# Performance work log

Hardware: AMD Instinct MI355X
Metric: run time of the kernel (lower is better)

## Reference

```python
import jax, jax.numpy as jnp
import numpy as np

D = 256      # dim
H = 8        # num_heads
HD = D // H  # head dim
P = 256      # patch_size
B = 4        # num clouds
L = 32768    # points per cloud (divisible by P)
N = B * L
MLP = int(D * 2.0)
PEH = max(32, D // 4)
EPS = 1e-5


def setup_inputs() -> dict:
    key = jax.random.key(0)
    ks = jax.random.split(key, 20)
    s = 0.02
    w = lambda k, shp: jax.random.normal(k, shp, jnp.float32) * s
    inp = {
        "feats": jax.random.normal(ks[0], (N, D), jnp.float32),
        "coord": jax.random.uniform(ks[1], (N, 3), jnp.float32),
        "lengths": jnp.full((B,), L, jnp.int32),
        # CoordPositionalEncoding: Linear(3,PEH) -> ReLU -> Linear(PEH,D)
        "pe_w1": w(ks[2], (3, PEH)), "pe_b1": jnp.zeros((PEH,), jnp.float32),
        "pe_w2": w(ks[3], (PEH, D)), "pe_b2": jnp.zeros((D,), jnp.float32),
        "pre_g": jnp.ones((D,), jnp.float32), "pre_b": jnp.zeros((D,), jnp.float32),
        # block: norm1 + MHA + norm2 + MLP
        "n1_g": jnp.ones((D,), jnp.float32), "n1_b": jnp.zeros((D,), jnp.float32),
        "wqkv": w(ks[4], (D, 3 * D)), "bqkv": jnp.zeros((3 * D,), jnp.float32),
        "wo": w(ks[5], (D, D)), "bo": jnp.zeros((D,), jnp.float32),
        "n2_g": jnp.ones((D,), jnp.float32), "n2_b": jnp.zeros((D,), jnp.float32),
        "m_w1": w(ks[6], (D, MLP)), "m_b1": jnp.zeros((MLP,), jnp.float32),
        "m_w2": w(ks[7], (MLP, D)), "m_b2": jnp.zeros((D,), jnp.float32),
        # global_gate: Linear(2D,D)->ReLU->Linear(D,D)->Sigmoid
        "gg_w1": w(ks[8], (2 * D, D)), "gg_b1": jnp.zeros((D,), jnp.float32),
        "gg_w2": w(ks[9], (D, D)), "gg_b2": jnp.zeros((D,), jnp.float32),
        # fuse: Linear(2D,D)->ReLU->Linear(D,D)
        "f_w1": w(ks[10], (2 * D, D)), "f_b1": jnp.zeros((D,), jnp.float32),
        "f_w2": w(ks[11], (D, D)), "f_b2": jnp.zeros((D,), jnp.float32),
    }
    return inp


def _ln(x, g, b):
    m = x.mean(-1, keepdims=True)
    v = jnp.mean((x - m) ** 2, -1, keepdims=True)
    return (x - m) * jax.lax.rsqrt(v + EPS) * g + b


def _sgca(feats, coord, lengths,
          pe_w1, pe_b1, pe_w2, pe_b2, pre_g, pre_b,
          n1_g, n1_b, wqkv, bqkv, wo, bo, n2_g, n2_b,
          m_w1, m_b1, m_w2, m_b2,
          gg_w1, gg_b1, gg_w2, gg_b2, f_w1, f_b1, f_w2, f_b2):
    Bn = lengths.shape[0]
    Ln = feats.shape[0] // Bn  # equal-length clouds

    def cloud(f, c):  # f: [L, D], c: [L, 3]
        # positional encoding (per-cloud centered / max-abs scaled coords)
        cc = c - c.mean(0, keepdims=True)
        scale = jnp.clip(jnp.abs(cc).max(0, keepdims=True), 1e-6)
        pe = jax.nn.relu((cc / scale) @ pe_w1 + pe_b1) @ pe_w2 + pe_b2
        x = _ln(f + pe, pre_g, pre_b)
        # serialization order from min-max normalized coords
        cn = c - c.min(0, keepdims=True)
        cn = cn / jnp.clip(cn.max(0, keepdims=True), 1e-6)
        key = cn[:, 0] + 2.17 * cn[:, 1] + 3.31 * cn[:, 2]
        order = jnp.argsort(key)
        xs = x[order].reshape(-1, P, D)  # [NP, P, D] block-diagonal windows
        # attention block (pre-norm MHA + residual)
        h = _ln(xs, n1_g, n1_b)
        qkv = h @ wqkv + bqkv
        q = qkv[..., :D].reshape(-1, P, H, HD)
        k = qkv[..., D:2 * D].reshape(-1, P, H, HD)
        v = qkv[..., 2 * D:].reshape(-1, P, H, HD)
        scores = jnp.einsum('nphd,nqhd->nhpq', q, k) / np.sqrt(HD).astype(np.float32)
        a = jax.nn.softmax(scores, axis=-1)
        o = jnp.einsum('nhpq,nqhd->nphd', a, v).reshape(-1, P, D)
        xs = xs + (o @ wo + bo)
        # MLP + residual
        xs = xs + (jax.nn.gelu(_ln(xs, n2_g, n2_b) @ m_w1 + m_b1, approximate=False) @ m_w2 + m_b2)
        # undo serialization
        xo = xs.reshape(-1, D)[jnp.argsort(order)]
        # global token gate/fuse
        gt = jnp.broadcast_to(xo.mean(0, keepdims=True), xo.shape)
        gate = jax.nn.sigmoid(jax.nn.relu(jnp.concatenate([f, gt], -1) @ gg_w1 + gg_b1) @ gg_w2 + gg_b2)
        fused = jax.nn.relu(jnp.concatenate([xo, gt], -1) @ f_w1 + f_b1) @ f_w2 + f_b2
        return f + gate * fused

    out = jax.vmap(cloud)(feats.reshape(Bn, Ln, D), coord.reshape(Bn, Ln, 3))
    return out.reshape(-1, D)


def reference(feats, coord, lengths,
              pe_w1, pe_b1, pe_w2, pe_b2, pre_g, pre_b,
              n1_g, n1_b, wqkv, bqkv, wo, bo, n2_g, n2_b,
              m_w1, m_b1, m_w2, m_b2,
              gg_w1, gg_b1, gg_w2, gg_b2, f_w1, f_b1, f_w2, f_b2):
    return _sgca(feats, coord, lengths,
                 pe_w1, pe_b1, pe_w2, pe_b2, pre_g, pre_b,
                 n1_g, n1_b, wqkv, bqkv, wo, bo, n2_g, n2_b,
                 m_w1, m_b1, m_w2, m_b2,
                 gg_w1, gg_b1, gg_w2, gg_b2, f_w1, f_b1, f_w2, f_b2)
```

## Files before the change

### kernel.cpp

```cpp
#include <hip/hip_runtime.h>
#include <hip/hip_bf16.h>
#include <math.h>

#define D_DIM 256
#define NHEAD 8
#define HDIM 32
#define PATCH 256
#define NCLOUD 4
#define LPC 32768
#define NTOT (NCLOUD * LPC)
#define MLPD 512
#define PEHID 64
#define LN_EPS 1e-5f
#define NCHUNK 4
#define CROWS (NTOT / NCHUNK)

typedef unsigned long long u64;
typedef unsigned short u16;
typedef short bf16x8 __attribute__((ext_vector_type(8)));
typedef float f32x4 __attribute__((ext_vector_type(4)));

__device__ __forceinline__ u16 f2bf(float x) {
  unsigned u = __float_as_uint(x);
  u += 0x7fffu + ((u >> 16) & 1u);
  return (u16)(u >> 16);
}
__device__ __forceinline__ float bf2f(u16 u) {
  return __uint_as_float(((unsigned)u) << 16);
}

__device__ __forceinline__ void gload_lds16(const u16* g, u16* l) {
  __builtin_amdgcn_global_load_lds((const __attribute__((address_space(1))) void*)g,
                                   (__attribute__((address_space(3))) void*)l, 16, 0, 0);
}

__global__ __launch_bounds__(256) void stats_kernel(const float* __restrict__ coord,
                                                    float* __restrict__ stats) {
  const int c = blockIdx.x, t = threadIdx.x;
  float sm[3] = {0.f, 0.f, 0.f};
  float mn[3] = {1e30f, 1e30f, 1e30f};
  float mx[3] = {-1e30f, -1e30f, -1e30f};
  const float* cp = coord + (size_t)c * LPC * 3;
  for (int i = t; i < LPC; i += 256) {
#pragma unroll
    for (int a = 0; a < 3; a++) {
      float v = cp[(size_t)i * 3 + a];
      sm[a] += v;
      mn[a] = fminf(mn[a], v);
      mx[a] = fmaxf(mx[a], v);
    }
  }
  __shared__ float sb[256];
  float rsum[3], rmn[3], rmx[3];
#pragma unroll
  for (int a = 0; a < 3; a++) {
    sb[t] = sm[a]; __syncthreads();
    for (int s = 128; s > 0; s >>= 1) { if (t < s) sb[t] += sb[t + s]; __syncthreads(); }
    rsum[a] = sb[0]; __syncthreads();
    sb[t] = mn[a]; __syncthreads();
    for (int s = 128; s > 0; s >>= 1) { if (t < s) sb[t] = fminf(sb[t], sb[t + s]); __syncthreads(); }
    rmn[a] = sb[0]; __syncthreads();
    sb[t] = mx[a]; __syncthreads();
    for (int s = 128; s > 0; s >>= 1) { if (t < s) sb[t] = fmaxf(sb[t], sb[t + s]); __syncthreads(); }
    rmx[a] = sb[0]; __syncthreads();
  }
  if (t == 0) {
    float* st = stats + c * 16;
#pragma unroll
    for (int a = 0; a < 3; a++) {
      float mean = rsum[a] / (float)LPC;
      st[a] = mean;
      st[3 + a] = fmaxf(fmaxf(rmx[a] - mean, mean - rmn[a]), 1e-6f);
      st[6 + a] = rmn[a];
      st[9 + a] = fmaxf(rmx[a] - rmn[a], 1e-6f);
    }
  }
}

__global__ __launch_bounds__(256) void key_kernel(const float* __restrict__ coord,
                                                  const float* __restrict__ stats,
                                                  u64* __restrict__ keys) {
#pragma clang fp contract(off)
  const int g = blockIdx.x * 256 + threadIdx.x;
  const int c = g >> 15;
  const float* st = stats + c * 16;
  float k0 = (coord[(size_t)g * 3 + 0] - st[6]) / st[9];
  float k1 = (coord[(size_t)g * 3 + 1] - st[7]) / st[10];
  float k2 = (coord[(size_t)g * 3 + 2] - st[8]) / st[11];
  float key = k0 + 2.17f * k1;
  key = key + 3.31f * k2;
  keys[g] = ((u64)__float_as_uint(key) << 32) | (unsigned)(g & (LPC - 1));
}

__global__ __launch_bounds__(1024) void sort_local_kernel(u64* __restrict__ keys) {
  __shared__ u64 s[4096];
  const int base = blockIdx.x * 4096;
  const int t = threadIdx.x;
  for (int i = t; i < 4096; i += 1024) s[i] = keys[base + i];
  __syncthreads();
  for (int k = 2; k <= 4096; k <<= 1) {
    for (int j = k >> 1; j > 0; j >>= 1) {
      for (int p = t; p < 2048; p += 1024) {
        int i = ((p & ~(j - 1)) << 1) | (p & (j - 1));
        int l = i | j;
        bool asc = (((base + i) & (LPC - 1)) & k) == 0;
        u64 a = s[i], bb = s[l];
        if (asc ? (a > bb) : (a < bb)) { s[i] = bb; s[l] = a; }
      }
      __syncthreads();
    }
  }
  for (int i = t; i < 4096; i += 1024) keys[base + i] = s[i];
}

__global__ __launch_bounds__(256) void sort_global_kernel(u64* __restrict__ keys, int k, int j) {
  int p = blockIdx.x * 256 + threadIdx.x;
  int i = ((p & ~(j - 1)) << 1) | (p & (j - 1));
  int l = i | j;
  bool asc = ((i & (LPC - 1)) & k) == 0;
  u64 a = keys[i], b = keys[l];
  if (asc ? (a > b) : (a < b)) { keys[i] = b; keys[l] = a; }
}

__global__ __launch_bounds__(1024) void sort_finish_kernel(u64* __restrict__ keys, int k) {
  __shared__ u64 s[4096];
  const int base = blockIdx.x * 4096;
  const int t = threadIdx.x;
  for (int i = t; i < 4096; i += 1024) s[i] = keys[base + i];
  __syncthreads();
  for (int j = 2048; j > 0; j >>= 1) {
    for (int p = t; p < 2048; p += 1024) {
      int i = ((p & ~(j - 1)) << 1) | (p & (j - 1));
      int l = i | j;
      bool asc = (((base + i) & (LPC - 1)) & k) == 0;
      u64 a = s[i], bb = s[l];
      if (asc ? (a > bb) : (a < bb)) { s[i] = bb; s[l] = a; }
    }
    __syncthreads();
  }
  for (int i = t; i < 4096; i += 1024) keys[base + i] = s[i];
}

__global__ __launch_bounds__(256) void rank_kernel(const u64* __restrict__ keys,
                                                   int* __restrict__ order,
                                                   int* __restrict__ rank) {
  const int g = blockIdx.x * 256 + threadIdx.x;
  const int src = (int)(unsigned)(keys[g] & 0xffffffffULL) + (g & ~(LPC - 1));
  order[g] = src;
  rank[src] = g;
}

__global__ __launch_bounds__(256) void wtrans_kernel(const float* __restrict__ src,
                                                     u16* __restrict__ dst, int R, int C) {
  __shared__ float t[32][33];
  const int bx = blockIdx.x * 32, by = blockIdx.y * 32;
  const int lc = threadIdx.x & 31, lr = threadIdx.x >> 5;
  for (int i = 0; i < 32; i += 8) t[lr + i][lc] = src[(size_t)(by + lr + i) * C + bx + lc];
  __syncthreads();
  for (int i = 0; i < 32; i += 8)
    dst[(size_t)(bx + lr + i) * R + by + lc] = f2bf(t[lc][lr + i]);
}

__global__ __launch_bounds__(256) void h_kernel(const float* __restrict__ coord,
                                                const float* __restrict__ stats,
                                                const float* __restrict__ pw1,
                                                const float* __restrict__ pb1,
                                                u16* __restrict__ H) {
  const int idx = blockIdx.x * 256 + threadIdx.x;
  const int row = idx >> 6, j = idx & 63;
  const int c = row >> 15;
  const float* st = stats + c * 16;
  float s0 = (coord[(size_t)row * 3 + 0] - st[0]) / st[3];
  float s1 = (coord[(size_t)row * 3 + 1] - st[1]) / st[4];
  float s2 = (coord[(size_t)row * 3 + 2] - st[2]) / st[5];
  float h = pb1[j] + s0 * pw1[j] + s1 * pw1[64 + j] + s2 * pw1[128 + j];
  H[idx] = f2bf(fmaxf(h, 0.f));
}

__global__ __launch_bounds__(256) void add_ln2_kernel(const float* __restrict__ feats,
                                                      const u16* __restrict__ pe,
                                                      const int* __restrict__ rank,
                                                      const float* __restrict__ g0,
                                                      const float* __restrict__ b0,
                                                      const float* __restrict__ g1,
                                                      const float* __restrict__ b1,
                                                      float* __restrict__ xs,
                                                      u16* __restrict__ ln1out) {
  const int row = blockIdx.x * 4 + (threadIdx.x >> 6);
  const int lane = threadIdx.x & 63;
  float4 f = *(const float4*)(feats + (size_t)row * 256 + lane * 4);
  ushort4 p = *(const ushort4*)(pe + (size_t)row * 256 + lane * 4);
  float v0 = f.x + bf2f(p.x), v1 = f.y + bf2f(p.y);
  float v2 = f.z + bf2f(p.z), v3 = f.w + bf2f(p.w);
  float s = v0 + v1 + v2 + v3;
#pragma unroll
  for (int o = 32; o > 0; o >>= 1) s += __shfl_xor(s, o);
  float mean = s * (1.f / 256.f);
  float d0 = v0 - mean, d1 = v1 - mean, d2 = v2 - mean, d3 = v3 - mean;
  float ss = d0 * d0 + d1 * d1 + d2 * d2 + d3 * d3;
#pragma unroll
  for (int o = 32; o > 0; o >>= 1) ss += __shfl_xor(ss, o);
  float inv = 1.f / sqrtf(ss * (1.f / 256.f) + LN_EPS);
  float4 gv = *(const float4*)(g0 + lane * 4);
  float4 bv = *(const float4*)(b0 + lane * 4);
  const int dst = rank[row];
  float y0 = d0 * inv * gv.x + bv.x, y1 = d1 * inv * gv.y + bv.y;
  float y2 = d2 * inv * gv.z + bv.z, y3 = d3 * inv * gv.w + bv.w;
  float4 o4 = {y0, y1, y2, y3};
  *(float4*)(xs + (size_t)dst * 256 + lane * 4) = o4;
  float s2s = y0 + y1 + y2 + y3;
#pragma unroll
  for (int o = 32; o > 0; o >>= 1) s2s += __shfl_xor(s2s, o);
  float mean2 = s2s * (1.f / 256.f);
  float e0 = y0 - mean2, e1 = y1 - mean2, e2 = y2 - mean2, e3 = y3 - mean2;
  float ss2 = e0 * e0 + e1 * e1 + e2 * e2 + e3 * e3;
#pragma unroll
  for (int o = 32; o > 0; o >>= 1) ss2 += __shfl_xor(ss2, o);
  float inv2 = 1.f / sqrtf(ss2 * (1.f / 256.f) + LN_EPS);
  float4 g1v = *(const float4*)(g1 + lane * 4);
  float4 b1v = *(const float4*)(b1 + lane * 4);
  ushort4 h4;
  h4.x = f2bf(e0 * inv2 * g1v.x + b1v.x); h4.y = f2bf(e1 * inv2 * g1v.y + b1v.y);
  h4.z = f2bf(e2 * inv2 * g1v.z + b1v.z); h4.w = f2bf(e3 * inv2 * g1v.w + b1v.w);
  *(ushort4*)(ln1out + (size_t)dst * 256 + lane * 4) = h4;
}

template <int K, int ACT, int MODE, bool EXTRA>
__global__ __launch_bounds__(256, 4) void mfma_gemm(const u16* __restrict__ A,
                                                    const u16* __restrict__ Wt,
                                                    const float* __restrict__ bias,
                                                    const float* __restrict__ extra,
                                                    void* __restrict__ Cout, int Ko) {
  __shared__ __align__(16) u16 Al[128 * 32];
  __shared__ __align__(16) u16 Bl[128 * 32];
  const int tid = threadIdx.x;
  const int lane = tid & 63, wave = tid >> 6;
  const int wr = wave >> 1, wc = wave & 1;
  const int l15 = lane & 15, l4 = lane >> 4;
  const size_t row0 = (size_t)blockIdx.y * 128;
  const int col0 = blockIdx.x * 128;
  const int q0 = wave * 64 + lane;
  const int q1 = q0 + 256;
  const u16* gA0 = A + (row0 + (q0 >> 2)) * K + (q0 & 3) * 8;
  const u16* gA1 = A + (row0 + (q1 >> 2)) * K + (q1 & 3) * 8;
  const u16* gB0 = Wt + (size_t)(col0 + (q0 >> 2)) * K + (q0 & 3) * 8;
  const u16* gB1 = Wt + (size_t)(col0 + (q1 >> 2)) * K + (q1 & 3) * 8;
  u16* lA0 = Al + wave * 512;
  u16* lA1 = Al + 2048 + wave * 512;
  u16* lB0 = Bl + wave * 512;
  u16* lB1 = Bl + 2048 + wave * 512;
  f32x4 acc[4][4];
#pragma unroll
  for (int i = 0; i < 4; i++)
#pragma unroll
    for (int j = 0; j < 4; j++) acc[i][j] = f32x4{0.f, 0.f, 0.f, 0.f};
#pragma unroll 1
  for (int k0 = 0; k0 < K; k0 += 32) {
    gload_lds16(gA0 + k0, lA0);
    gload_lds16(gA1 + k0, lA1);
    gload_lds16(gB0 + k0, lB0);
    gload_lds16(gB1 + k0, lB1);
    __syncthreads();
    bf16x8 af[4], bfr[4];
#pragma unroll
    for (int rb = 0; rb < 4; rb++)
      af[rb] = *(const bf16x8*)&Al[(wr * 64 + rb * 16 + l15) * 32 + l4 * 8];
#pragma unroll
    for (int cb = 0; cb < 4; cb++)
      bfr[cb] = *(const bf16x8*)&Bl[(wc * 64 + cb * 16 + l15) * 32 + l4 * 8];
#pragma unroll
    for (int rb = 0; rb < 4; rb++)
#pragma unroll
      for (int cb = 0; cb < 4; cb++)
        acc[rb][cb] = __builtin_amdgcn_mfma_f32_16x16x32_bf16(af[rb], bfr[cb], acc[rb][cb], 0, 0, 0);
    __syncthreads();
  }
#pragma unroll
  for (int rb = 0; rb < 4; rb++)
#pragma unroll
    for (int cb = 0; cb < 4; cb++)
#pragma unroll
      for (int r = 0; r < 4; r++) {
        size_t row = row0 + wr * 64 + rb * 16 + l4 * 4 + r;
        int col = col0 + wc * 64 + cb * 16 + l15;
        float v = acc[rb][cb][r] + bias[col];
        if (EXTRA) v += extra[((int)(row >> 15)) * 256 + col];
        if (ACT == 1) v = fmaxf(v, 0.f);
        else if (ACT == 2) v = 0.5f * v * (1.f + erff(v * 0.70710678118654752440f));
        else if (ACT == 3) v = 1.f / (1.f + __expf(-v));
        size_t o = row * (size_t)Ko + col;
        if (MODE == 0) ((float*)Cout)[o] = v;
        else if (MODE == 1) ((float*)Cout)[o] += v;
        else ((u16*)Cout)[o] = f2bf(v);
      }
}

template <int K, int EPI>
__global__ __launch_bounds__(256, 3) void mfma_row_gemm(const u16* __restrict__ A,
                                                        const u16* __restrict__ Wt,
                                                        const float* __restrict__ bias,
                                                        float* __restrict__ xs,
                                                        u16* __restrict__ hout,
                                                        const int* __restrict__ order,
                                                        const float* __restrict__ g,
                                                        const float* __restrict__ b) {
  __shared__ __align__(16) u16 Al[64 * 32];
  __shared__ __align__(16) u16 Bl[256 * 32];
  __shared__ float reds[2][4][64];
  const int tid = threadIdx.x;
  const int lane = tid & 63, wave = tid >> 6;
  const int l15 = lane & 15, l4 = lane >> 4;
  const size_t row0 = (size_t)blockIdx.x * 64;
  const u16* gA = A + (row0 + (tid >> 2)) * K + (tid & 3) * 8;
  u16* lA = Al + wave * 512;
  const u16* gB[4];
  u16* lB[4];
#pragma unroll
  for (int s = 0; s < 4; s++) {
    int q = s * 256 + tid;
    gB[s] = Wt + (size_t)(q >> 2) * K + (q & 3) * 8;
    lB[s] = Bl + s * 2048 + wave * 512;
  }
  f32x4 acc[4][4];
#pragma unroll
  for (int i = 0; i < 4; i++)
#pragma unroll
    for (int j = 0; j < 4; j++) acc[i][j] = f32x4{0.f, 0.f, 0.f, 0.f};
#pragma unroll 1
  for (int k0 = 0; k0 < K; k0 += 32) {
    gload_lds16(gA + k0, lA);
#pragma unroll
    for (int s = 0; s < 4; s++) gload_lds16(gB[s] + k0, lB[s]);
    __syncthreads();
    bf16x8 af[4], bfr[4];
#pragma unroll
    for (int rb = 0; rb < 4; rb++)
      af[rb] = *(const bf16x8*)&Al[(rb * 16 + l15) * 32 + l4 * 8];
#pragma unroll
    for (int cb = 0; cb < 4; cb++)
      bfr[cb] = *(const bf16x8*)&Bl[(wave * 64 + cb * 16 + l15) * 32 + l4 * 8];
#pragma unroll
    for (int rb = 0; rb < 4; rb++)
#pragma unroll
      for (int cb = 0; cb < 4; cb++)
        acc[rb][cb] = __builtin_amdgcn_mfma_f32_16x16x32_bf16(af[rb], bfr[cb], acc[rb][cb], 0, 0, 0);
    __syncthreads();
  }
#pragma unroll
  for (int rb = 0; rb < 4; rb++)
#pragma unroll
    for (int cb = 0; cb < 4; cb++)
#pragma unroll
      for (int r = 0; r < 4; r++) {
        size_t row = row0 + rb * 16 + l4 * 4 + r;
        int col = wave * 64 + cb * 16 + l15;
        size_t o = row * 256 + col;
        float t = xs[o] + acc[rb][cb][r] + bias[col];
        xs[o] = t;
        acc[rb][cb][r] = t;
      }
  if (EPI == 1) {
    float ps[4][4];
#pragma unroll
    for (int rb = 0; rb < 4; rb++)
#pragma unroll
      for (int r = 0; r < 4; r++) {
        float v = acc[rb][0][r] + acc[rb][1][r] + acc[rb][2][r] + acc[rb][3][r];
#pragma unroll
        for (int oo = 1; oo < 16; oo <<= 1) v += __shfl_xor(v, oo);
        ps[rb][r] = v;
      }
    if (l15 == 0)
#pragma unroll
      for (int rb = 0; rb < 4; rb++)
#pragma unroll
        for (int r = 0; r < 4; r++) reds[0][wave][rb * 16 + l4 * 4 + r] = ps[rb][r];
    __syncthreads();
    float mean[4][4];
#pragma unroll
    for (int rb = 0; rb < 4; rb++)
#pragma unroll
      for (int r = 0; r < 4; r++) {
        int ri = rb * 16 + l4 * 4 + r;
        mean[rb][r] = (reds[0][0][ri] + reds[0][1][ri] + reds[0][2][ri] + reds[0][3][ri]) *
                      (1.f / 256.f);
      }
#pragma unroll
    for (int rb = 0; rb < 4; rb++)
#pragma unroll
      for (int r = 0; r < 4; r++) {
        float d0 = acc[rb][0][r] - mean[rb][r], d1 = acc[rb][1][r] - mean[rb][r];
        float d2 = acc[rb][2][r] - mean[rb][r], d3 = acc[rb][3][r] - mean[rb][r];
        float v = d0 * d0 + d1 * d1 + d2 * d2 + d3 * d3;
#pragma unroll
        for (int oo = 1; oo < 16; oo <<= 1) v += __shfl_xor(v, oo);
        ps[rb][r] = v;
      }
    if (l15 == 0)
#pragma unroll
      for (int rb = 0; rb < 4; rb++)
#pragma unroll
        for (int r = 0; r < 4; r++) reds[1][wave][rb * 16 + l4 * 4 + r] = ps[rb][r];
    __syncthreads();
#pragma unroll
    for (int rb = 0; rb < 4; rb++)
#pragma unroll
      for (int r = 0; r < 4; r++) {
        int ri = rb * 16 + l4 * 4 + r;
        float var = (reds[1][0][ri] + reds[1][1][ri] + reds[1][2][ri] + reds[1][3][ri]) *
                    (1.f / 256.f);
        float inv = 1.f / sqrtf(var + LN_EPS);
        size_t row = row0 + ri;
#pragma unroll
        for (int cb = 0; cb < 4; cb++) {
          int col = wave * 64 + cb * 16 + l15;
          hout[row * 256 + col] =
              f2bf((acc[rb][cb][r] - mean[rb][r]) * inv * g[col] + b[col]);
        }
      }
  } else {
#pragma unroll
    for (int rb = 0; rb < 4; rb++)
#pragma unroll
      for (int r = 0; r < 4; r++) {
        size_t row = row0 + rb * 16 + l4 * 4 + r;
        size_t dst = (size_t)order[row];
#pragma unroll
        for (int cb = 0; cb < 4; cb++) {
          int col = wave * 64 + cb * 16 + l15;
          hout[dst * 256 + col] = f2bf(acc[rb][cb][r]);
        }
      }
  }
}

__global__ __launch_bounds__(256, 2) void tail_kernel(
    const float* __restrict__ feats, const u16* __restrict__ xobf,
    const u16* __restrict__ ggw1T, const u16* __restrict__ fw1T,
    const u16* __restrict__ ggw2T, const u16* __restrict__ fw2T,
    const float* __restrict__ ggt, const float* __restrict__ fgt,
    const float* __restrict__ b1g, const float* __restrict__ b1f,
    const float* __restrict__ b2g, const float* __restrict__ b2f,
    float* __restrict__ out) {
  __shared__ __align__(16) u16 g1l[32 * 264];
  __shared__ __align__(16) u16 u1l[32 * 264];
  __shared__ __align__(16) u16 Bst[2][256 * 32];
  __shared__ __align__(16) u16 Ast[2][32 * 32];
  const int tid = threadIdx.x;
  const int lane = tid & 63, wave = tid >> 6;
  const int l15 = lane & 15, l4 = lane >> 4;
  const size_t row0 = (size_t)blockIdx.x * 32;
  const int cloud = (int)(row0 >> 15);
  f32x4 acc[2][4];

#pragma unroll
  for (int i = 0; i < 2; i++)
#pragma unroll
    for (int j = 0; j < 4; j++) acc[i][j] = f32x4{0.f, 0.f, 0.f, 0.f};
#pragma unroll 1
  for (int k0 = 0; k0 < 256; k0 += 64) {
    __syncthreads();
#pragma unroll
    for (int h = 0; h < 2; h++) {
#pragma unroll
      for (int s = 0; s < 4; s++) {
        int q = s * 256 + tid;
        gload_lds16(ggw1T + (size_t)(q >> 2) * 256 + k0 + h * 32 + (q & 3) * 8,
                    &Bst[h][0] + s * 2048 + wave * 512);
      }
      int r = tid >> 3, c4 = (tid & 7) * 4;
      float4 v = *(const float4*)(feats + (row0 + r) * 256 + k0 + h * 32 + c4);
      ushort4 o4; o4.x = f2bf(v.x); o4.y = f2bf(v.y); o4.z = f2bf(v.z); o4.w = f2bf(v.w);
      *(ushort4*)&Ast[h][r * 32 + c4] = o4;
    }
    __syncthreads();
#pragma unroll
    for (int h = 0; h < 2; h++) {
      bf16x8 af[2];
#pragma unroll
      for (int rb = 0; rb < 2; rb++)
        af[rb] = *(const bf16x8*)&Ast[h][(rb * 16 + l15) * 32 + l4 * 8];
#pragma unroll
      for (int cb = 0; cb < 4; cb++) {
        bf16x8 bf = *(const bf16x8*)&Bst[h][(wave * 64 + cb * 16 + l15) * 32 + l4 * 8];
#pragma unroll
        for (int rb = 0; rb < 2; rb++)
          acc[rb][cb] = __builtin_amdgcn_mfma_f32_16x16x32_bf16(af[rb], bf, acc[rb][cb], 0, 0, 0);
      }
    }
  }
#pragma unroll
  for (int rb = 0; rb < 2; rb++)
#pragma unroll
    for (int cb = 0; cb < 4; cb++)
#pragma unroll
      for (int r = 0; r < 4; r++) {
        int row = rb * 16 + l4 * 4 + r;
        int col = wave * 64 + cb * 16 + l15;
        float v = acc[rb][cb][r] + b1g[col] + ggt[cloud * 256 + col];
        g1l[row * 264 + col] = f2bf(fmaxf(v, 0.f));
      }
#pragma unroll
  for (int i = 0; i < 2; i++)
#pragma unroll
    for (int j = 0; j < 4; j++) acc[i][j] = f32x4{0.f, 0.f, 0.f, 0.f};
#pragma unroll 1
  for (int k0 = 0; k0 < 256; k0 += 64) {
    __syncthreads();
#pragma unroll
    for (int h = 0; h < 2; h++) {
#pragma unroll
      for (int s = 0; s < 4; s++) {
        int q = s * 256 + tid;
        gload_lds16(fw1T + (size_t)(q >> 2) * 256 + k0 + h * 32 + (q & 3) * 8,
                    &Bst[h][0] + s * 2048 + wave * 512);
      }
      if (tid < 128) {
        int q = tid;
        gload_lds16(xobf + (row0 + (q >> 2)) * 256 + k0 + h * 32 + (q & 3) * 8,
                    &Ast[h][0] + wave * 512);
      }
    }
    __syncthreads();
#pragma unroll
    for (int h = 0; h < 2; h++) {
      bf16x8 af[2];
#pragma unroll
      for (int rb = 0; rb < 2; rb++)
        af[rb] = *(const bf16x8*)&Ast[h][(rb * 16 + l15) * 32 + l4 * 8];
#pragma unroll
      for (int cb = 0; cb < 4; cb++) {
        bf16x8 bf = *(const bf16x8*)&Bst[h][(wave * 64 + cb * 16 + l15) * 32 + l4 * 8];
#pragma unroll
        for (int rb = 0; rb < 2; rb++)
          acc[rb][cb] = __builtin_amdgcn_mfma_f32_16x16x32_bf16(af[rb], bf, acc[rb][cb], 0, 0, 0);
      }
    }
  }
#pragma unroll
  for (int rb = 0; rb < 2; rb++)
#pragma unroll
    for (int cb = 0; cb < 4; cb++)
#pragma unroll
      for (int r = 0; r < 4; r++) {
        int row = rb * 16 + l4 * 4 + r;
        int col = wave * 64 + cb * 16 + l15;
        float v = acc[rb][cb][r] + b1f[col] + fgt[cloud * 256 + col];
        u1l[row * 264 + col] = f2bf(fmaxf(v, 0.f));
      }
#pragma unroll
  for (int i = 0; i < 2; i++)
#pragma unroll
    for (int j = 0; j < 4; j++) acc[i][j] = f32x4{0.f, 0.f, 0.f, 0.f};
#pragma unroll 1
  for (int k0 = 0; k0 < 256; k0 += 64) {
    __syncthreads();
#pragma unroll
    for (int h = 0; h < 2; h++)
#pragma unroll
      for (int s = 0; s < 4; s++) {
        int q = s * 256 + tid;
        gload_lds16(ggw2T + (size_t)(q >> 2) * 256 + k0 + h * 32 + (q & 3) * 8,
                    &Bst[h][0] + s * 2048 + wave * 512);
      }
    __syncthreads();
#pragma unroll
    for (int h = 0; h < 2; h++) {
      bf16x8 af[2];
#pragma unroll
      for (int rb = 0; rb < 2; rb++)
        af[rb] = *(const bf16x8*)&g1l[(rb * 16 + l15) * 264 + k0 + h * 32 + l4 * 8];
#pragma unroll
      for (int cb = 0; cb < 4; cb++) {
        bf16x8 bf = *(const bf16x8*)&Bst[h][(wave * 64 + cb * 16 + l15) * 32 + l4 * 8];
#pragma unroll
        for (int rb = 0; rb < 2; rb++)
          acc[rb][cb] = __builtin_amdgcn_mfma_f32_16x16x32_bf16(af[rb], bf, acc[rb][cb], 0, 0, 0);
      }
    }
  }
  float sg[2][4][4];
#pragma unroll
  for (int rb = 0; rb < 2; rb++)
#pragma unroll
    for (int cb = 0; cb < 4; cb++)
#pragma unroll
      for (int r = 0; r < 4; r++) {
        int col = wave * 64 + cb * 16 + l15;
        sg[rb][cb][r] = 1.f / (1.f + __expf(-(acc[rb][cb][r] + b2g[col])));
      }
#pragma unroll
  for (int i = 0; i < 2; i++)
#pragma unroll
    for (int j = 0; j < 4; j++) acc[i][j] = f32x4{0.f, 0.f, 0.f, 0.f};
#pragma unroll 1
  for (int k0 = 0; k0 < 256; k0 += 64) {
    __syncthreads();
#pragma unroll
    for (int h = 0; h < 2; h++)
#pragma unroll
      for (int s = 0; s < 4; s++) {
        int q = s * 256 + tid;
        gload_lds16(fw2T + (size_t)(q >> 2) * 256 + k0 + h * 32 + (q & 3) * 8,
                    &Bst[h][0] + s * 2048 + wave * 512);
      }
    __syncthreads();
#pragma unroll
    for (int h = 0; h < 2; h++) {
      bf16x8 af[2];
#pragma unroll
      for (int rb = 0; rb < 2; rb++)
        af[rb] = *(const bf16x8*)&u1l[(rb * 16 + l15) * 264 + k0 + h * 32 + l4 * 8];
#pragma unroll
      for (int cb = 0; cb < 4; cb++) {
        bf16x8 bf = *(const bf16x8*)&Bst[h][(wave * 64 + cb * 16 + l15) * 32 + l4 * 8];
#pragma unroll
        for (int rb = 0; rb < 2; rb++)
          acc[rb][cb] = __builtin_amdgcn_mfma_f32_16x16x32_bf16(af[rb], bf, acc[rb][cb], 0, 0, 0);
      }
    }
  }
#pragma unroll
  for (int rb = 0; rb < 2; rb++)
#pragma unroll
    for (int cb = 0; cb < 4; cb++)
#pragma unroll
      for (int r = 0; r < 4; r++) {
        size_t row = row0 + rb * 16 + l4 * 4 + r;
        int col = wave * 64 + cb * 16 + l15;
        size_t o = row * 256 + col;
        out[o] = feats[o] + sg[rb][cb][r] * (acc[rb][cb][r] + b2f[col]);
      }
}

__global__ __launch_bounds__(256, 3) void attn_mfma_kernel(const u16* __restrict__ qkv,
                                                           u16* __restrict__ ao) {
  __shared__ __align__(16) u16 VT[32 * 264];
  __shared__ __align__(16) u16 Pl[4][16 * 264];
  const int w = blockIdx.x, h = blockIdx.y;
  const int tid = threadIdx.x;
  const int lane = tid & 63, wave = tid >> 6;
  const int l15 = lane & 15, l4 = lane >> 4;
  const size_t base = (size_t)w * PATCH;
  {
    const u16* vrow = qkv + (base + tid) * 768 + 512 + h * HDIM;
#pragma unroll
    for (int d4 = 0; d4 < 8; d4++) {
      ushort4 v4 = *(const ushort4*)(vrow + d4 * 4);
      VT[(d4 * 4 + 0) * 264 + tid] = v4.x;
      VT[(d4 * 4 + 1) * 264 + tid] = v4.y;
      VT[(d4 * 4 + 2) * 264 + tid] = v4.z;
      VT[(d4 * 4 + 3) * 264 + tid] = v4.w;
    }
  }
  __syncthreads();
  u16* Pw = &Pl[wave][0];
  const float scale = 0.17677669529663687f;
  const f32x4 zero = {0.f, 0.f, 0.f, 0.f};
  for (int qt = 0; qt < 4; qt++) {
    const int qbase = wave * 64 + qt * 16;
    bf16x8 qf = *(const bf16x8*)(qkv + (base + qbase + l15) * 768 + h * HDIM + l4 * 8);
    f32x4 s[16];
#pragma unroll
    for (int kt = 0; kt < 16; kt++) {
      bf16x8 kf = *(const bf16x8*)(qkv + (base + kt * 16 + l15) * 768 + 256 + h * HDIM + l4 * 8);
      s[kt] = __builtin_amdgcn_mfma_f32_16x16x32_bf16(kf, qf, zero, 0, 0, 0);
    }
    float m = -1e30f;
#pragma unroll
    for (int kt = 0; kt < 16; kt++)
#pragma unroll
      for (int r = 0; r < 4; r++) { s[kt][r] *= scale; m = fmaxf(m, s[kt][r]); }
    m = fmaxf(m, __shfl_xor(m, 16));
    m = fmaxf(m, __shfl_xor(m, 32));
    float lsum = 0.f;
#pragma unroll
    for (int kt = 0; kt < 16; kt++) {
      float p0 = __expf(s[kt][0] - m), p1 = __expf(s[kt][1] - m);
      float p2 = __expf(s[kt][2] - m), p3 = __expf(s[kt][3] - m);
      lsum += (p0 + p1) + (p2 + p3);
      ushort4 pw4;
      pw4.x = f2bf(p0); pw4.y = f2bf(p1); pw4.z = f2bf(p2); pw4.w = f2bf(p3);
      *(ushort4*)&Pw[l15 * 264 + kt * 16 + l4 * 4] = pw4;
    }
    lsum += __shfl_xor(lsum, 16);
    lsum += __shfl_xor(lsum, 32);
    f32x4 o0 = zero, o1 = zero;
#pragma unroll
    for (int kc = 0; kc < 8; kc++) {
      bf16x8 pf = *(const bf16x8*)&Pw[l15 * 264 + kc * 32 + l4 * 8];
      bf16x8 va = *(const bf16x8*)&VT[l15 * 264 + kc * 32 + l4 * 8];
      bf16x8 vb = *(const bf16x8*)&VT[(16 + l15) * 264 + kc * 32 + l4 * 8];
      o0 = __builtin_amdgcn_mfma_f32_16x16x32_bf16(va, pf, o0, 0, 0, 0);
      o1 = __builtin_amdgcn_mfma_f32_16x16x32_bf16(vb, pf, o1, 0, 0, 0);
    }
    float inv = 1.f / lsum;
    u16* op = ao + (base + qbase + l15) * D_DIM + h * HDIM;
    ushort4 w0, w1;
    w0.x = f2bf(o0[0] * inv); w0.y = f2bf(o0[1] * inv);
    w0.z = f2bf(o0[2] * inv); w0.w = f2bf(o0[3] * inv);
    w1.x = f2bf(o1[0] * inv); w1.y = f2bf(o1[1] * inv);
    w1.z = f2bf(o1[2] * inv); w1.w = f2bf(o1[3] * inv);
    *(ushort4*)(op + l4 * 4) = w0;
    *(ushort4*)(op + 16 + l4 * 4) = w1;
  }
}

__global__ __launch_bounds__(256) void gt_partial_kernel(const float* __restrict__ xs,
                                                         float* __restrict__ part) {
  const int s = blockIdx.x, c = blockIdx.y;
  const int t = threadIdx.x;
  float acc = 0.f;
  const size_t base = (size_t)c * LPC + (size_t)s * 256;
  for (int r = 0; r < 256; r++) acc += xs[(base + r) * D_DIM + t];
  part[(size_t)(c * 128 + s) * D_DIM + t] = acc;
}

__global__ __launch_bounds__(256) void gt_reduce_kernel(const float* __restrict__ part,
                                                        float* __restrict__ gt) {
  const int c = blockIdx.x, t = threadIdx.x;
  float s = 0.f;
  for (int i = 0; i < 128; i++) s += part[(size_t)(c * 128 + i) * D_DIM + t];
  gt[c * D_DIM + t] = s * (1.f / (float)LPC);
}

__global__ __launch_bounds__(256) void pervec_kernel(const float* __restrict__ gt,
                                                     const float* __restrict__ ggw1,
                                                     const float* __restrict__ fw1,
                                                     float* __restrict__ ggt,
                                                     float* __restrict__ fgt) {
  const int c = blockIdx.x, which = blockIdx.y;
  const int t = threadIdx.x;
  const float* W = which ? fw1 : ggw1;
  float* o = which ? fgt : ggt;
  __shared__ float g[D_DIM];
  g[t] = gt[c * D_DIM + t];
  __syncthreads();
  float acc = 0.f;
#pragma unroll 8
  for (int k = 0; k < D_DIM; k++) acc += g[k] * W[(size_t)(256 + k) * D_DIM + t];
  o[c * D_DIM + t] = acc;
}

extern "C" void kernel_launch(void* const* d_in, const int* in_sizes, int n_in,
                              void* d_out, int out_size, void* d_ws, size_t ws_size,
                              hipStream_t stream) {
  const float* feats = (const float*)d_in[0];
  const float* coord = (const float*)d_in[1];
  const float* pe_w1 = (const float*)d_in[3];
  const float* pe_b1 = (const float*)d_in[4];
  const float* pe_w2 = (const float*)d_in[5];
  const float* pe_b2 = (const float*)d_in[6];
  const float* pre_g = (const float*)d_in[7];
  const float* pre_b = (const float*)d_in[8];
  const float* n1_g = (const float*)d_in[9];
  const float* n1_b = (const float*)d_in[10];
  const float* wqkv = (const float*)d_in[11];
  const float* bqkv = (const float*)d_in[12];
  const float* wo = (const float*)d_in[13];
  const float* bo = (const float*)d_in[14];
  const float* n2_g = (const float*)d_in[15];
  const float* n2_b = (const float*)d_in[16];
  const float* m_w1 = (const float*)d_in[17];
  const float* m_b1 = (const float*)d_in[18];
  const float* m_w2 = (const float*)d_in[19];
  const float* m_b2 = (const float*)d_in[20];
  const float* gg_w1 = (const float*)d_in[21];
  const float* gg_b1 = (const float*)d_in[22];
  const float* gg_w2 = (const float*)d_in[23];
  const float* gg_b2 = (const float*)d_in[24];
  const float* f_w1 = (const float*)d_in[25];
  const float* f_b1 = (const float*)d_in[26];
  const float* f_w2 = (const float*)d_in[27];
  const float* f_b2 = (const float*)d_in[28];
  float* out = (float*)d_out;

  char* ws = (char*)d_ws;
  float* xs = (float*)(ws);
  u16* hbuf = (u16*)(ws + 134217728);
  u16* pebuf = (u16*)(ws + 201326592);
  u16* qkvchunk = (u16*)(ws + 201326592);
  u16* aochunk = (u16*)(ws + 251658240);
  u16* tbuf = (u16*)(ws + 268435456);
  u16* Hbuf = (u16*)(ws + 268435456);
  u16* xobf = (u16*)(ws + 201326592);
  size_t off = 301989888;
  u64* keybuf = (u64*)(ws + off); off += (size_t)NTOT * 8;
  int* orderbuf = (int*)(ws + off); off += (size_t)NTOT * 4;
  int* rankbuf = (int*)(ws + off); off += (size_t)NTOT * 4;
  float* statsbuf = (float*)(ws + off); off += 4096;
  float* gtpart = (float*)(ws + off); off += (size_t)NCLOUD * 128 * D_DIM * 4;
  float* gtbuf = (float*)(ws + off); off += 4096;
  float* ggtbuf = (float*)(ws + off); off += 4096;
  float* fgtbuf = (float*)(ws + off); off += 4096;
  u16* wqkvT = (u16*)(ws + off); off += 768 * 256 * 2;
  u16* woT = (u16*)(ws + off); off += 256 * 256 * 2;
  u16* mw1T = (u16*)(ws + off); off += 512 * 256 * 2;
  u16* mw2T = (u16*)(ws + off); off += 256 * 512 * 2;
  u16* ggw1T = (u16*)(ws + off); off += 256 * 256 * 2;
  u16* ggw2T = (u16*)(ws + off); off += 256 * 256 * 2;
  u16* fw1T = (u16*)(ws + off); off += 256 * 256 * 2;
  u16* fw2T = (u16*)(ws + off); off += 256 * 256 * 2;
  u16* pw2T = (u16*)(ws + off); off += 64 * 256 * 2;

  stats_kernel<<<NCLOUD, 256, 0, stream>>>(coord, statsbuf);
  key_kernel<<<NTOT / 256, 256, 0, stream>>>(coord, statsbuf, keybuf);
  sort_local_kernel<<<NTOT / 4096, 1024, 0, stream>>>(keybuf);
  for (int k = 8192; k <= 32768; k <<= 1) {
    for (int j = k >> 1; j >= 4096; j >>= 1)
      sort_global_kernel<<<NTOT / 512, 256, 0, stream>>>(keybuf, k, j);
    sort_finish_kernel<<<NTOT / 4096, 1024, 0, stream>>>(keybuf, k);
  }
  rank_kernel<<<NTOT / 256, 256, 0, stream>>>(keybuf, orderbuf, rankbuf);
  wtrans_kernel<<<dim3(24, 8), 256, 0, stream>>>(wqkv, wqkvT, 256, 768);
  wtrans_kernel<<<dim3(8, 8), 256, 0, stream>>>(wo, woT, 256, 256);
  wtrans_kernel<<<dim3(16, 8), 256, 0, stream>>>(m_w1, mw1T, 256, 512);
  wtrans_kernel<<<dim3(8, 16), 256, 0, stream>>>(m_w2, mw2T, 512, 256);
  wtrans_kernel<<<dim3(8, 8), 256, 0, stream>>>(gg_w1, ggw1T, 256, 256);
  wtrans_kernel<<<dim3(8, 8), 256, 0, stream>>>(gg_w2, ggw2T, 256, 256);
  wtrans_kernel<<<dim3(8, 8), 256, 0, stream>>>(f_w1, fw1T, 256, 256);
  wtrans_kernel<<<dim3(8, 8), 256, 0, stream>>>(f_w2, fw2T, 256, 256);
  wtrans_kernel<<<dim3(8, 2), 256, 0, stream>>>(pe_w2, pw2T, 64, 256);
  h_kernel<<<NTOT * 64 / 256, 256, 0, stream>>>(coord, statsbuf, pe_w1, pe_b1, Hbuf);
  mfma_gemm<64, 0, 2, false><<<dim3(2, NTOT / 128), 256, 0, stream>>>(
      Hbuf, pw2T, pe_b2, nullptr, pebuf, 256);
  add_ln2_kernel<<<NTOT / 4, 256, 0, stream>>>(feats, pebuf, rankbuf, pre_g, pre_b,
                                               n1_g, n1_b, xs, hbuf);
  for (int ch = 0; ch < NCHUNK; ch++) {
    const size_t ro = (size_t)ch * CROWS;
    mfma_gemm<256, 0, 2, false><<<dim3(6, CROWS / 128), 256, 0, stream>>>(
        hbuf + ro * 256, wqkvT, bqkv, nullptr, qkvchunk, 768);
    attn_mfma_kernel<<<dim3(CROWS / PATCH, NHEAD), 256, 0, stream>>>(qkvchunk, aochunk);
    mfma_row_gemm<256, 1><<<CROWS / 64, 256, 0, stream>>>(
        aochunk, woT, bo, xs + ro * 256, hbuf + ro * 256, nullptr, n2_g, n2_b);
  }
  for (int ch = 0; ch < NCHUNK; ch++) {
    const size_t ro = (size_t)ch * CROWS;
    mfma_gemm<256, 2, 2, false><<<dim3(MLPD / 128, CROWS / 128), 256, 0, stream>>>(
        hbuf + ro * 256, mw1T, m_b1, nullptr, tbuf, 512);
    mfma_row_gemm<512, 2><<<CROWS / 64, 256, 0, stream>>>(
        tbuf, mw2T, m_b2, xs + ro * 256, xobf, orderbuf + ro, nullptr, nullptr);
  }
  gt_partial_kernel<<<dim3(128, NCLOUD), 256, 0, stream>>>(xs, gtpart);
  gt_reduce_kernel<<<NCLOUD, 256, 0, stream>>>(gtpart, gtbuf);
  pervec_kernel<<<dim3(NCLOUD, 2), 256, 0, stream>>>(gtbuf, gg_w1, f_w1, ggtbuf, fgtbuf);
  tail_kernel<<<NTOT / 32, 256, 0, stream>>>(feats, xobf, ggw1T, fw1T, ggw2T, fw2T,
                                             ggtbuf, fgtbuf, gg_b1, f_b1, gg_b2, f_b2, out);
  (void)in_sizes; (void)n_in; (void)out_size; (void)ws_size;
}
```

Measured before the change: 1.345 ms.

## Fuse PE GEMM with LayerNorms, enlarge sort tiles, fold global-mean partials into MLP epilogue

The positional-encoding GEMM now runs inside a row kernel whose epilogue adds feats and the bias and applies both LayerNorms before scattering, so the bf16 PE intermediate is never written or re-read. The bitonic sort uses 8192-element shared-memory tiles, which removes several global merge passes and kernel launches. Column sums for the global token are computed in the MLP output GEMM epilogue, replacing the separate pass over xs. In exchange the sort kernels use 64KB of LDS per block, and the fused PE kernel does strided scalar epilogue stores and carries extra register pressure.

Measured after the change: 1.353 ms. No clear change (+0.5%).

```diff
diff --git a/kernel.cpp b/kernel.cpp
--- a/kernel.cpp
+++ b/kernel.cpp
@@ -92,15 +92,15 @@
   keys[g] = ((u64)__float_as_uint(key) << 32) | (unsigned)(g & (LPC - 1));
 }
 
-__global__ __launch_bounds__(1024) void sort_local_kernel(u64* __restrict__ keys) {
-  __shared__ u64 s[4096];
-  const int base = blockIdx.x * 4096;
+__global__ __launch_bounds__(1024) void sort_local8_kernel(u64* __restrict__ keys) {
+  __shared__ u64 s[8192];
+  const int base = blockIdx.x * 8192;
   const int t = threadIdx.x;
-  for (int i = t; i < 4096; i += 1024) s[i] = keys[base + i];
-  __syncthreads();
-  for (int k = 2; k <= 4096; k <<= 1) {
+  for (int i = t; i < 8192; i += 1024) s[i] = keys[base + i];
+  __syncthreads();
+  for (int k = 2; k <= 8192; k <<= 1) {
     for (int j = k >> 1; j > 0; j >>= 1) {
-      for (int p = t; p < 2048; p += 1024) {
+      for (int p = t; p < 4096; p += 1024) {
         int i = ((p & ~(j - 1)) << 1) | (p & (j - 1));
         int l = i | j;
         bool asc = (((base + i) & (LPC - 1)) & k) == 0;
@@ -110,7 +110,7 @@
       __syncthreads();
     }
   }
-  for (int i = t; i < 4096; i += 1024) keys[base + i] = s[i];
+  for (int i = t; i < 8192; i += 1024) keys[base + i] = s[i];
 }
 
 __global__ __launch_bounds__(256) void sort_global_kernel(u64* __restrict__ keys, int k, int j) {
@@ -122,14 +122,14 @@
   if (asc ? (a > b) : (a < b)) { keys[i] = b; keys[l] = a; }
 }
 
-__global__ __launch_bounds__(1024) void sort_finish_kernel(u64* __restrict__ keys, int k) {
-  __shared__ u64 s[4096];
-  const int base = blockIdx.x * 4096;
+__global__ __launch_bounds__(1024) void sort_finish8_kernel(u64* __restrict__ keys, int k) {
+  __shared__ u64 s[8192];
+  const int base = blockIdx.x * 8192;
   const int t = threadIdx.x;
-  for (int i = t; i < 4096; i += 1024) s[i] = keys[base + i];
-  __syncthreads();
-  for (int j = 2048; j > 0; j >>= 1) {
-    for (int p = t; p < 2048; p += 1024) {
+  for (int i = t; i < 8192; i += 1024) s[i] = keys[base + i];
+  __syncthreads();
+  for (int j = 4096; j > 0; j >>= 1) {
+    for (int p = t; p < 4096; p += 1024) {
       int i = ((p & ~(j - 1)) << 1) | (p & (j - 1));
       int l = i | j;
       bool asc = (((base + i) & (LPC - 1)) & k) == 0;
@@ -138,7 +138,7 @@
     }
     __syncthreads();
   }
-  for (int i = t; i < 4096; i += 1024) keys[base + i] = s[i];
+  for (int i = t; i < 8192; i += 1024) keys[base + i] = s[i];
 }
 
 __global__ __launch_bounds__(256) void rank_kernel(const u64* __restrict__ keys,
@@ -177,52 +177,182 @@
   H[idx] = f2bf(fmaxf(h, 0.f));
 }
 
-__global__ __launch_bounds__(256) void add_ln2_kernel(const float* __restrict__ feats,
-                                                      const u16* __restrict__ pe,
-                                                      const int* __restrict__ rank,
-                                                      const float* __restrict__ g0,
-                                                      const float* __restrict__ b0,
-                                                      const float* __restrict__ g1,
-                                                      const float* __restrict__ b1,
-                                                      float* __restrict__ xs,
-                                                      u16* __restrict__ ln1out) {
-  const int row = blockIdx.x * 4 + (threadIdx.x >> 6);
-  const int lane = threadIdx.x & 63;
-  float4 f = *(const float4*)(feats + (size_t)row * 256 + lane * 4);
-  ushort4 p = *(const ushort4*)(pe + (size_t)row * 256 + lane * 4);
-  float v0 = f.x + bf2f(p.x), v1 = f.y + bf2f(p.y);
-  float v2 = f.z + bf2f(p.z), v3 = f.w + bf2f(p.w);
-  float s = v0 + v1 + v2 + v3;
-#pragma unroll
-  for (int o = 32; o > 0; o >>= 1) s += __shfl_xor(s, o);
-  float mean = s * (1.f / 256.f);
-  float d0 = v0 - mean, d1 = v1 - mean, d2 = v2 - mean, d3 = v3 - mean;
-  float ss = d0 * d0 + d1 * d1 + d2 * d2 + d3 * d3;
-#pragma unroll
-  for (int o = 32; o > 0; o >>= 1) ss += __shfl_xor(ss, o);
-  float inv = 1.f / sqrtf(ss * (1.f / 256.f) + LN_EPS);
-  float4 gv = *(const float4*)(g0 + lane * 4);
-  float4 bv = *(const float4*)(b0 + lane * 4);
-  const int dst = rank[row];
-  float y0 = d0 * inv * gv.x + bv.x, y1 = d1 * inv * gv.y + bv.y;
-  float y2 = d2 * inv * gv.z + bv.z, y3 = d3 * inv * gv.w + bv.w;
-  float4 o4 = {y0, y1, y2, y3};
-  *(float4*)(xs + (size_t)dst * 256 + lane * 4) = o4;
-  float s2s = y0 + y1 + y2 + y3;
-#pragma unroll
-  for (int o = 32; o > 0; o >>= 1) s2s += __shfl_xor(s2s, o);
-  float mean2 = s2s * (1.f / 256.f);
-  float e0 = y0 - mean2, e1 = y1 - mean2, e2 = y2 - mean2, e3 = y3 - mean2;
-  float ss2 = e0 * e0 + e1 * e1 + e2 * e2 + e3 * e3;
-#pragma unroll
-  for (int o = 32; o > 0; o >>= 1) ss2 += __shfl_xor(ss2, o);
-  float inv2 = 1.f / sqrtf(ss2 * (1.f / 256.f) + LN_EPS);
-  float4 g1v = *(const float4*)(g1 + lane * 4);
-  float4 b1v = *(const float4*)(b1 + lane * 4);
-  ushort4 h4;
-  h4.x = f2bf(e0 * inv2 * g1v.x + b1v.x); h4.y = f2bf(e1 * inv2 * g1v.y + b1v.y);
-  h4.z = f2bf(e2 * inv2 * g1v.z + b1v.z); h4.w = f2bf(e3 * inv2 * g1v.w + b1v.w);
-  *(ushort4*)(ln1out + (size_t)dst * 256 + lane * 4) = h4;
+__global__ __launch_bounds__(256, 3) void pe_row_kernel(
+    const u16* __restrict__ H, const u16* __restrict__ pw2T,
+    const float* __restrict__ pb2, const float* __restrict__ feats,
+    const int* __restrict__ rank,
+    const float* __restrict__ g0, const float* __restrict__ b0,
+    const float* __restrict__ g1, const float* __restrict__ b1,
+    float* __restrict__ xs, u16* __restrict__ ln1out) {
+  __shared__ __align__(16) u16 Al[64 * 32];
+  __shared__ __align__(16) u16 Bl[256 * 32];
+  __shared__ float reds[2][4][64];
+  const int tid = threadIdx.x;
+  const int lane = tid & 63, wave = tid >> 6;
+  const int l15 = lane & 15, l4 = lane >> 4;
+  const size_t row0 = (size_t)blockIdx.x * 64;
+  const u16* gA = H + (row0 + (tid >> 2)) * 64 + (tid & 3) * 8;
+  u16* lA = Al + wave * 512;
+  const u16* gB[4];
+  u16* lB[4];
+#pragma unroll
+  for (int s = 0; s < 4; s++) {
+    int q = s * 256 + tid;
+    gB[s] = pw2T + (size_t)(q >> 2) * 64 + (q & 3) * 8;
+    lB[s] = Bl + s * 2048 + wave * 512;
+  }
+  f32x4 acc[4][4];
+#pragma unroll
+  for (int i = 0; i < 4; i++)
+#pragma unroll
+    for (int j = 0; j < 4; j++) acc[i][j] = f32x4{0.f, 0.f, 0.f, 0.f};
+#pragma unroll 1
+  for (int k0 = 0; k0 < 64; k0 += 32) {
+    gload_lds16(gA + k0, lA);
+#pragma unroll
+    for (int s = 0; s < 4; s++) gload_lds16(gB[s] + k0, lB[s]);
+    __syncthreads();
+    bf16x8 af[4], bfr[4];
+#pragma unroll
+    for (int rb = 0; rb < 4; rb++)
+      af[rb] = *(const bf16x8*)&Al[(rb * 16 + l15) * 32 + l4 * 8];
+#pragma unroll
+    for (int cb = 0; cb < 4; cb++)
+      bfr[cb] = *(const bf16x8*)&Bl[(wave * 64 + cb * 16 + l15) * 32 + l4 * 8];
+#pragma unroll
+    for (int rb = 0; rb < 4; rb++)
+#pragma unroll
+      for (int cb = 0; cb < 4; cb++)
+        acc[rb][cb] = __builtin_amdgcn_mfma_f32_16x16x32_bf16(af[rb], bfr[cb], acc[rb][cb], 0, 0, 0);
+    __syncthreads();
+  }
+#pragma unroll
+  for (int rb = 0; rb < 4; rb++)
+#pragma unroll
+    for (int cb = 0; cb < 4; cb++)
+#pragma unroll
+      for (int r = 0; r < 4; r++) {
+        size_t row = row0 + rb * 16 + l4 * 4 + r;
+        int col = wave * 64 + cb * 16 + l15;
+        acc[rb][cb][r] = feats[row * 256 + col] + acc[rb][cb][r] + pb2[col];
+      }
+  float ps[4][4], mean[4][4];
+#pragma unroll
+  for (int rb = 0; rb < 4; rb++)
+#pragma unroll
+    for (int r = 0; r < 4; r++) {
+      float v = acc[rb][0][r] + acc[rb][1][r] + acc[rb][2][r] + acc[rb][3][r];
+#pragma unroll
+      for (int oo = 1; oo < 16; oo <<= 1) v += __shfl_xor(v, oo);
+      ps[rb][r] = v;
+    }
+  if (l15 == 0)
+#pragma unroll
+    for (int rb = 0; rb < 4; rb++)
+#pragma unroll
+      for (int r = 0; r < 4; r++) reds[0][wave][rb * 16 + l4 * 4 + r] = ps[rb][r];
+  __syncthreads();
+#pragma unroll
+  for (int rb = 0; rb < 4; rb++)
+#pragma unroll
+    for (int r = 0; r < 4; r++) {
+      int ri = rb * 16 + l4 * 4 + r;
+      mean[rb][r] = (reds[0][0][ri] + reds[0][1][ri] + reds[0][2][ri] + reds[0][3][ri]) *
+                    (1.f / 256.f);
+    }
+#pragma unroll
+  for (int rb = 0; rb < 4; rb++)
+#pragma unroll
+    for (int r = 0; r < 4; r++) {
+      float d0 = acc[rb][0][r] - mean[rb][r], d1 = acc[rb][1][r] - mean[rb][r];
+      float d2 = acc[rb][2][r] - mean[rb][r], d3 = acc[rb][3][r] - mean[rb][r];
+      float v = d0 * d0 + d1 * d1 + d2 * d2 + d3 * d3;
+#pragma unroll
+      for (int oo = 1; oo < 16; oo <<= 1) v += __shfl_xor(v, oo);
+      ps[rb][r] = v;
+    }
+  if (l15 == 0)
+#pragma unroll
+    for (int rb = 0; rb < 4; rb++)
+#pragma unroll
+      for (int r = 0; r < 4; r++) reds[1][wave][rb * 16 + l4 * 4 + r] = ps[rb][r];
+  __syncthreads();
+#pragma unroll
+  for (int rb = 0; rb < 4; rb++)
+#pragma unroll
+    for (int r = 0; r < 4; r++) {
+      int ri = rb * 16 + l4 * 4 + r;
+      float var = (reds[1][0][ri] + reds[1][1][ri] + reds[1][2][ri] + reds[1][3][ri]) *
+                  (1.f / 256.f);
+      float inv = 1.f / sqrtf(var + LN_EPS);
+      size_t row = row0 + ri;
+      size_t dst = (size_t)rank[row];
+#pragma unroll
+      for (int cb = 0; cb < 4; cb++) {
+        int col = wave * 64 + cb * 16 + l15;
+        float y = (acc[rb][cb][r] - mean[rb][r]) * inv * g0[col] + b0[col];
+        acc[rb][cb][r] = y;
+        xs[dst * 256 + col] = y;
+      }
+    }
+#pragma unroll
+  for (int rb = 0; rb < 4; rb++)
+#pragma unroll
+    for (int r = 0; r < 4; r++) {
+      float v = acc[rb][0][r] + acc[rb][1][r] + acc[rb][2][r] + acc[rb][3][r];
+#pragma unroll
+      for (int oo = 1; oo < 16; oo <<= 1) v += __shfl_xor(v, oo);
+      ps[rb][r] = v;
+    }
+  __syncthreads();
+  if (l15 == 0)
+#pragma unroll
+    for (int rb = 0; rb < 4; rb++)
+#pragma unroll
+      for (int r = 0; r < 4; r++) reds[0][wave][rb * 16 + l4 * 4 + r] = ps[rb][r];
+  __syncthreads();
+#pragma unroll
+  for (int rb = 0; rb < 4; rb++)
+#pragma unroll
+    for (int r = 0; r < 4; r++) {
+      int ri = rb * 16 + l4 * 4 + r;
+      mean[rb][r] = (reds[0][0][ri] + reds[0][1][ri] + reds[0][2][ri] + reds[0][3][ri]) *
+                    (1.f / 256.f);
+    }
+#pragma unroll
+  for (int rb = 0; rb < 4; rb++)
+#pragma unroll
+    for (int r = 0; r < 4; r++) {
+      float d0 = acc[rb][0][r] - mean[rb][r], d1 = acc[rb][1][r] - mean[rb][r];
+      float d2 = acc[rb][2][r] - mean[rb][r], d3 = acc[rb][3][r] - mean[rb][r];
+      float v = d0 * d0 + d1 * d1 + d2 * d2 + d3 * d3;
+#pragma unroll
+      for (int oo = 1; oo < 16; oo <<= 1) v += __shfl_xor(v, oo);
+      ps[rb][r] = v;
+    }
+  if (l15 == 0)
+#pragma unroll
+    for (int rb = 0; rb < 4; rb++)
+#pragma unroll
+      for (int r = 0; r < 4; r++) reds[1][wave][rb * 16 + l4 * 4 + r] = ps[rb][r];
+  __syncthreads();
+#pragma unroll
+  for (int rb = 0; rb < 4; rb++)
+#pragma unroll
+    for (int r = 0; r < 4; r++) {
+      int ri = rb * 16 + l4 * 4 + r;
+      float var = (reds[1][0][ri] + reds[1][1][ri] + reds[1][2][ri] + reds[1][3][ri]) *
+                  (1.f / 256.f);
+      float inv = 1.f / sqrtf(var + LN_EPS);
+      size_t row = row0 + ri;
+      size_t dst = (size_t)rank[row];
+#pragma unroll
+      for (int cb = 0; cb < 4; cb++) {
+        int col = wave * 64 + cb * 16 + l15;
+        ln1out[dst * 256 + col] =
+            f2bf((acc[rb][cb][r] - mean[rb][r]) * inv * g1[col] + b1[col]);
+      }
+    }
 }
 
 template <int K, int ACT, int MODE, bool EXTRA>
@@ -303,7 +433,9 @@
                                                         u16* __restrict__ hout,
                                                         const int* __restrict__ order,
                                                         const float* __restrict__ g,
-                                                        const float* __restrict__ b) {
+                                                        const float* __restrict__ b,
+                                                        float* __restrict__ gtpart,
+                                                        int pbase) {
   __shared__ __align__(16) u16 Al[64 * 32];
   __shared__ __align__(16) u16 Bl[256 * 32];
   __shared__ float reds[2][4][64];
@@ -419,6 +551,18 @@
         }
       }
   } else {
+#pragma unroll
+    for (int cb = 0; cb < 4; cb++) {
+      float cs = 0.f;
+#pragma unroll
+      for (int rb = 0; rb < 4; rb++)
+#pragma unroll
+        for (int r = 0; r < 4; r++) cs += acc[rb][cb][r];
+      cs += __shfl_xor(cs, 16);
+      cs += __shfl_xor(cs, 32);
+      if (l4 == 0)
+        gtpart[(size_t)(pbase + blockIdx.x) * 256 + wave * 64 + cb * 16 + l15] = cs;
+    }
 #pragma unroll
     for (int rb = 0; rb < 4; rb++)
 #pragma unroll
@@ -706,22 +850,19 @@
   }
 }
 
-__global__ __launch_bounds__(256) void gt_partial_kernel(const float* __restrict__ xs,
-                                                         float* __restrict__ part) {
-  const int s = blockIdx.x, c = blockIdx.y;
-  const int t = threadIdx.x;
-  float acc = 0.f;
-  const size_t base = (size_t)c * LPC + (size_t)s * 256;
-  for (int r = 0; r < 256; r++) acc += xs[(base + r) * D_DIM + t];
-  part[(size_t)(c * 128 + s) * D_DIM + t] = acc;
-}
-
-__global__ __launch_bounds__(256) void gt_reduce_kernel(const float* __restrict__ part,
-                                                        float* __restrict__ gt) {
-  const int c = blockIdx.x, t = threadIdx.x;
+__global__ __launch_bounds__(1024) void gt_reduce_kernel(const float* __restrict__ part,
+                                                         float* __restrict__ gt) {
+  const int c = blockIdx.x;
+  const int col = threadIdx.x & 255, q = threadIdx.x >> 8;
+  __shared__ float red[4][256];
   float s = 0.f;
-  for (int i = 0; i < 128; i++) s += part[(size_t)(c * 128 + i) * D_DIM + t];
-  gt[c * D_DIM + t] = s * (1.f / (float)LPC);
+  for (int i = q * 128; i < q * 128 + 128; i++)
+    s += part[(size_t)(c * 512 + i) * 256 + col];
+  red[q][col] = s;
+  __syncthreads();
+  if (q == 0)
+    gt[c * 256 + col] =
+        (red[0][col] + red[1][col] + red[2][col] + red[3][col]) * (1.f / (float)LPC);
 }
 
 __global__ __launch_bounds__(256) void pervec_kernel(const float* __restrict__ gt,
@@ -778,7 +919,6 @@
   char* ws = (char*)d_ws;
   float* xs = (float*)(ws);
   u16* hbuf = (u16*)(ws + 134217728);
-  u16* pebuf = (u16*)(ws + 201326592);
   u16* qkvchunk = (u16*)(ws + 201326592);
   u16* aochunk = (u16*)(ws + 251658240);
   u16* tbuf = (u16*)(ws + 268435456);
@@ -789,7 +929,7 @@
   int* orderbuf = (int*)(ws + off); off += (size_t)NTOT * 4;
   int* rankbuf = (int*)(ws + off); off += (size_t)NTOT * 4;
   float* statsbuf = (float*)(ws + off); off += 4096;
-  float* gtpart = (float*)(ws + off); off += (size_t)NCLOUD * 128 * D_DIM * 4;
+  float* gtpart = (float*)(ws + off); off += (size_t)(NTOT / 64) * 256 * 4;
   float* gtbuf = (float*)(ws + off); off += 4096;
   float* ggtbuf = (float*)(ws + off); off += 4096;
   float* fgtbuf = (float*)(ws + off); off += 4096;
@@ -805,12 +945,12 @@
 
   stats_kernel<<<NCLOUD, 256, 0, stream>>>(coord, statsbuf);
   key_kernel<<<NTOT / 256, 256, 0, stream>>>(coord, statsbuf, keybuf);
-  sort_local_kernel<<<NTOT / 4096, 1024, 0, stream>>>(keybuf);
-  for (int k = 8192; k <= 32768; k <<= 1) {
-    for (int j = k >> 1; j >= 4096; j >>= 1)
-      sort_global_kernel<<<NTOT / 512, 256, 0, stream>>>(keybuf, k, j);
-    sort_finish_kernel<<<NTOT / 4096, 1024, 0, stream>>>(keybuf, k);
-  }
+  sort_local8_kernel<<<NTOT / 8192, 1024, 0, stream>>>(keybuf);
+  sort_global_kernel<<<NTOT / 512, 256, 0, stream>>>(keybuf, 16384, 8192);
+  sort_finish8_kernel<<<NTOT / 8192, 1024, 0, stream>>>(keybuf, 16384);
+  sort_global_kernel<<<NTOT / 512, 256, 0, stream>>>(keybuf, 32768, 16384);
+  sort_global_kernel<<<NTOT / 512, 256, 0, stream>>>(keybuf, 32768, 8192);
+  sort_finish8_kernel<<<NTOT / 8192, 1024, 0, stream>>>(keybuf, 32768);
   rank_kernel<<<NTOT / 256, 256, 0, stream>>>(keybuf, orderbuf, rankbuf);
   wtrans_kernel<<<dim3(24, 8), 256, 0, stream>>>(wqkv, wqkvT, 256, 768);
   wtrans_kernel<<<dim3(8, 8), 256, 0, stream>>>(wo, woT, 256, 256);
@@ -822,27 +962,25 @@
   wtrans_kernel<<<dim3(8, 8), 256, 0, stream>>>(f_w2, fw2T, 256, 256);
   wtrans_kernel<<<dim3(8, 2), 256, 0, stream>>>(pe_w2, pw2T, 64, 256);
   h_kernel<<<NTOT * 64 / 256, 256, 0, stream>>>(coord, statsbuf, pe_w1, pe_b1, Hbuf);
-  mfma_gemm<64, 0, 2, false><<<dim3(2, NTOT / 128), 256, 0, stream>>>(
-      Hbuf, pw2T, pe_b2, nullptr, pebuf, 256);
-  add_ln2_kernel<<<NTOT / 4, 256, 0, stream>>>(feats, pebuf, rankbuf, pre_g, pre_b,
-                                               n1_g, n1_b, xs, hbuf);
+  pe_row_kernel<<<NTOT / 64, 256, 0, stream>>>(Hbuf, pw2T, pe_b2, feats, rankbuf, pre_g,
+                                               pre_b, n1_g, n1_b, xs, hbuf);
   for (int ch = 0; ch < NCHUNK; ch++) {
     const size_t ro = (size_t)ch * CROWS;
     mfma_gemm<256, 0, 2, false><<<dim3(6, CROWS / 128), 256, 0, stream>>>(
         hbuf + ro * 256, wqkvT, bqkv, nullptr, qkvchunk, 768);
     attn_mfma_kernel<<<dim3(CROWS / PATCH, NHEAD), 256, 0, stream>>>(qkvchunk, aochunk);
     mfma_row_gemm<256, 1><<<CROWS / 64, 256, 0, stream>>>(
-        aochunk, woT, bo, xs + ro * 256, hbuf + ro * 256, nullptr, n2_g, n2_b);
+        aochunk, woT, bo, xs + ro * 256, hbuf + ro * 256, nullptr, n2_g, n2_b, nullptr, 0);
   }
   for (int ch = 0; ch < NCHUNK; ch++) {
     const size_t ro = (size_t)ch * CROWS;
     mfma_gemm<256, 2, 2, false><<<dim3(MLPD / 128, CROWS / 128), 256, 0, stream>>>(
         hbuf + ro * 256, mw1T, m_b1, nullptr, tbuf, 512);
     mfma_row_gemm<512, 2><<<CROWS / 64, 256, 0, stream>>>(
-        tbuf, mw2T, m_b2, xs + ro * 256, xobf, orderbuf + ro, nullptr, nullptr);
-  }
-  gt_partial_kernel<<<dim3(128, NCLOUD), 256, 0, stream>>>(xs, gtpart);
-  gt_reduce_kernel<<<NCLOUD, 256, 0, stream>>>(gtpart, gtbuf);
+        tbuf, mw2T, m_b2, xs + ro * 256, xobf, orderbuf + ro, nullptr, nullptr, gtpart,
+        ch * (CROWS / 64));
+  }
+  gt_reduce_kernel<<<NCLOUD, 1024, 0, stream>>>(gtpart, gtbuf);
   pervec_kernel<<<dim3(NCLOUD, 2), 256, 0, stream>>>(gtbuf, gg_w1, f_w1, ggtbuf, fgtbuf);
   tail_kernel<<<NTOT / 32, 256, 0, stream>>>(feats, xobf, ggw1T, fw1T, ggw2T, fw2T,
                                              ggtbuf, fgtbuf, gg_b1, f_b1, gg_b2, f_b2, out);
```
